# Kernel tuning notes

Hardware: AMD Instinct MI355X
Metric: run time of the kernel (lower is better)

The kernel has to match this reference:

```python
import jax, jax.numpy as jnp
import numpy as np

B, S, D, H, P = 2, 2048, 512, 8, 10  # batch, seq, d_model, heads, max_relative_position
DH = D // H
SCALE = float(np.sqrt(D))  # module uses sqrt(d_model) in relative branch


def _rel_indices(len_q, len_k, max_rel):
    rq = jnp.arange(len_q)
    rk = jnp.arange(len_k)
    dist = rk[None, :] - rq[:, None]
    return jnp.clip(dist, -max_rel, max_rel) + max_rel  # [len_q, len_k]


def setup_inputs() -> dict:
    key = jax.random.key(0)
    ks = jax.random.split(key, 12)
    init = lambda k, shp, s=0.02: (jax.random.normal(k, shp, dtype=jnp.float32) * s)
    return {
        "q": jax.random.normal(ks[0], (B, S, D), dtype=jnp.float32),
        "k": jax.random.normal(ks[1], (B, S, D), dtype=jnp.float32),
        "v": jax.random.normal(ks[2], (B, S, D), dtype=jnp.float32),
        "mask": jnp.ones((1, 1, S, S), dtype=jnp.int32),  # no-op in original (masked_fill result discarded)
        "Wq": init(ks[3], (D, D)), "bq": init(ks[4], (D,)),
        "Wk": init(ks[5], (D, D)), "bk": init(ks[6], (D,)),
        "Wv": init(ks[7], (D, D)), "bv": init(ks[8], (D,)),
        "W0": init(ks[9], (D, D)), "b0": init(ks[10], (D,)),
        "rel_k_table": init(ks[11], (2 * P + 1, DH), 0.02),
        "rel_v_table": init(jax.random.fold_in(key, 99), (2 * P + 1, DH), 0.02),
    }


def reference(q, k, v, mask, Wq, bq, Wk, bk, Wv, bv, W0, b0, rel_k_table, rel_v_table):
    # Projections (nn.Linear equivalent with weight stored as [in, out])
    query = q @ Wq + bq  # [B,S,D]
    key_ = k @ Wk + bk
    value = v @ Wv + bv

    qh = query.reshape(B, S, H, DH)  # [B,S,H,DH]
    kh = key_.reshape(B, S, H, DH)
    vh = value.reshape(B, S, H, DH)

    idx = _rel_indices(S, S, P)              # [S,S]
    rel_k = rel_k_table[idx]                 # [S,S,DH]
    rel_v = rel_v_table[idx]                 # [S,S,DH]

    normal_scores = jnp.einsum("bqhd,bkhd->bhqk", qh, kh)
    rel_scores = jnp.einsum("bqhd,qkd->bhqk", qh, rel_k)
    # NOTE: original relative branch applies NO softmax; mask is a no-op (masked_fill not in-place)
    scores = (normal_scores + rel_scores) / SCALE  # [B,H,S,S]

    weight1 = jnp.einsum("bhqk,bkhd->bhqd", scores, vh)
    weight2 = jnp.einsum("bhqk,qkd->bhqd", scores, rel_v)
    x = (weight1 + weight2).transpose(0, 2, 1, 3).reshape(B, S, D)
    return x @ W0 + b0
```

## Files before the change

kernel.cpp:

```cpp
#include <hip/hip_runtime.h>
#include <hip/hip_bf16.h>


typedef __attribute__((ext_vector_type(8)))  short  short8;
typedef __attribute__((ext_vector_type(4)))  short  short4v;
typedef __attribute__((ext_vector_type(4)))  int    int4v;
typedef __attribute__((ext_vector_type(16))) float  f32x16;
typedef __attribute__((ext_vector_type(8)))  __bf16 bf16x8;

#define DEV static __device__ __forceinline__

constexpr float INV_SCALE = 0.044194173824159216f;

DEV unsigned short f2bs(float f){ __hip_bfloat16 h = __float2bfloat16(f); unsigned short u; __builtin_memcpy(&u,&h,2); return u; }
DEV short f2b(float f){ return (short)f2bs(f); }
DEV int   pk2(float a, float b){ return (int)((unsigned)f2bs(a) | ((unsigned)f2bs(b) << 16)); }
DEV bf16x8 ld8s(const short* p){ return __builtin_bit_cast(bf16x8, *(const short8*)p); }
DEV f32x16 z16(){ f32x16 z;
#pragma unroll
  for (int i=0;i<16;++i) z[i]=0.f;
  return z; }
DEV f32x16 mfma32(bf16x8 a, bf16x8 b, f32x16 c){ return __builtin_amdgcn_mfma_f32_32x32x16_bf16(a,b,c,0,0,0); }

struct WtArgs { const float* W[4]; short* O[4]; };

__global__ __launch_bounds__(256) void wt_kernel(WtArgs args){
  const float* W = args.W[blockIdx.z];
  short* O = args.O[blockIdx.z];
  const int kt = blockIdx.x*64, nt = blockIdx.y*64;
  __shared__ float t[64][65];
  const int tid = threadIdx.x;
#pragma unroll
  for (int p=0;p<4;++p){
    int idx = p*1024 + tid*4; int r = idx>>6, c = idx&63;
    float4 v = *(const float4*)(W + (size_t)(kt+r)*512 + nt + c);
    t[r][c]=v.x; t[r][c+1]=v.y; t[r][c+2]=v.z; t[r][c+3]=v.w;
  }
  __syncthreads();
#pragma unroll
  for (int p=0;p<4;++p){
    int idx = p*1024 + tid*4; int n = idx>>6, k = idx&63;
    short4v o = { f2b(t[k][n]), f2b(t[k+1][n]), f2b(t[k+2][n]), f2b(t[k+3][n]) };
    *(short4v*)(O + (size_t)(nt+n)*512 + kt + k) = o;
  }
}

template<bool AF32, bool OUTB16>
DEV void gemm_body(const void* A, const short* BT, const float* bias, void* C,
                   int m0, int n0, short* Alds, short* Blds){
  const int tid = threadIdx.x, lane = tid&63, wid = tid>>6, lo5 = lane&31, hi = lane>>5;
  f32x16 acc0 = z16(), acc1 = z16();
  for (int kt=0; kt<8; ++kt){
    const int k0 = kt*64;
    __syncthreads();
    {
      const int rr = tid>>3, c = tid&7;
#pragma unroll
      for (int p=0;p<4;++p){
        int row = p*32 + rr;
        short8 v;
        if (AF32){
          const float* ap = (const float*)A + (size_t)(m0+row)*512 + k0 + c*8;
          float4 x = *(const float4*)ap; float4 y = *(const float4*)(ap+4);
          v = short8{ f2b(x.x),f2b(x.y),f2b(x.z),f2b(x.w), f2b(y.x),f2b(y.y),f2b(y.z),f2b(y.w) };
        } else {
          v = *(const short8*)((const short*)A + (size_t)(m0+row)*512 + k0 + c*8);
        }
        *(short8*)&Alds[row*64 + ((c ^ (row&7))*8)] = v;
      }
#pragma unroll
      for (int p=0;p<2;++p){
        int row = p*32 + rr;
        short8 v = *(const short8*)(BT + (size_t)(n0+row)*512 + k0 + c*8);
        *(short8*)&Blds[row*64 + ((c ^ (row&7))*8)] = v;
      }
    }
    __syncthreads();
#pragma unroll
    for (int da=0; da<4; ++da){
      const int arow = wid*32 + lo5;
      bf16x8 af = ld8s(&Alds[arow*64 + (((2*da+hi) ^ (arow&7))*8)]);
      const int b0r = lo5, b1r = 32+lo5;
      bf16x8 bf0 = ld8s(&Blds[b0r*64 + (((2*da+hi) ^ (b0r&7))*8)]);
      bf16x8 bf1 = ld8s(&Blds[b1r*64 + (((2*da+hi) ^ (b1r&7))*8)]);
      acc0 = mfma32(af, bf0, acc0);
      acc1 = mfma32(af, bf1, acc1);
    }
  }
  const float bv0 = bias[n0 + lo5], bv1 = bias[n0 + 32 + lo5];
#pragma unroll
  for (int r=0;r<16;++r){
    const int m = m0 + wid*32 + (r&3) + 8*(r>>2) + 4*hi;
    const float v0 = acc0[r] + bv0, v1 = acc1[r] + bv1;
    if (OUTB16){
      ((short*)C)[(size_t)m*512 + n0 + lo5]      = f2b(v0);
      ((short*)C)[(size_t)m*512 + n0 + 32 + lo5] = f2b(v1);
    } else {
      ((float*)C)[(size_t)m*512 + n0 + lo5]      = v0;
      ((float*)C)[(size_t)m*512 + n0 + 32 + lo5] = v1;
    }
  }
}

struct ProjArgs { const float* A[3]; const short* BT[3]; const float* bias[3]; short* C[3]; };

__global__ __launch_bounds__(256) void proj_gemm(ProjArgs args){
  __shared__ short Alds[128*64];
  __shared__ short Blds[64*64];
  const int z = blockIdx.z;
  gemm_body<true,true>(args.A[z], args.BT[z], args.bias[z], args.C[z],
                       blockIdx.x*128, blockIdx.y*64, Alds, Blds);
}

__global__ __launch_bounds__(256) void out_gemm(const short* A, const short* BT, const float* bias, float* C){
  __shared__ short Alds[128*64];
  __shared__ short Blds[64*64];
  gemm_body<false,false>(A, BT, bias, C, blockIdx.x*128, blockIdx.y*64, Alds, Blds);
}

__global__ __launch_bounds__(256) void vt_kernel(const short* Vp, short* Vt){
  const int bh = blockIdx.y, s0 = blockIdx.x*64;
  const int b = bh>>3, h = bh&7;
  __shared__ short t[64][72];
  const int tid = threadIdx.x;
#pragma unroll
  for (int p=0;p<2;++p){
    int row = p*32 + (tid>>3), cc = (tid&7)*8;
    short8 v = *(const short8*)(Vp + (size_t)(b*2048 + s0 + row)*512 + h*64 + cc);
#pragma unroll
    for (int i=0;i<8;++i) t[row][cc+i] = v[i];
  }
  __syncthreads();
#pragma unroll
  for (int p=0;p<2;++p){
    int d = p*32 + (tid>>3), sc = (tid&7)*8;
    short8 o;
#pragma unroll
    for (int i=0;i<8;++i) o[i] = t[sc+i][d];
    *(short8*)(Vt + ((size_t)bh*64 + d)*2048 + s0 + sc) = o;
  }
}

__global__ __launch_bounds__(256) void attn_kernel(const short* Qp, const short* Kp, const short* Vt,
                                                   const float* relk_g, const float* relv_g, float* slab){
  const int qt = blockIdx.x, bh = blockIdx.y, ks = blockIdx.z;
  const int b = bh>>3, h = bh&7;
  const int tid = threadIdx.x, lane = tid&63, wid = tid>>6, lo5 = lane&31, hi = lane>>5;
  const int q0 = qt*128, qw = q0 + wid*32;

  __shared__ short Klds[64*64];
  __shared__ short Vl[64*64];
  __shared__ float Rq[128*21];
  __shared__ short CS[128*32];
  __shared__ short RVT[64*32];

  for (int i=tid; i<2048; i+=256) ((int*)CS)[i] = 0;
  for (int i=tid; i<2048; i+=256){
    int d = i>>5, j = i&31;
    RVT[d*32 + (j ^ ((d&3)<<3))] = (j<21) ? f2b(relv_g[j*64+d]) : (short)0;
  }

  bf16x8 qf[4];
  {
    const short* Qrow = Qp + (size_t)(b*2048 + qw + lo5)*512 + h*64 + hi*8;
#pragma unroll
    for (int da=0;da<4;++da) qf[da] = ld8s(Qrow + da*16);
  }

  {
    f32x16 rq = z16();
    const int jr = lo5 <= 20 ? lo5 : 20;
    const float* rp = relk_g + jr*64 + hi*8;
#pragma unroll
    for (int da=0;da<4;++da){
      const float* p = rp + da*16;
      float4 x = *(const float4*)p; float4 y = *(const float4*)(p+4);
      short8 rb = { f2b(x.x),f2b(x.y),f2b(x.z),f2b(x.w), f2b(y.x),f2b(y.y),f2b(y.z),f2b(y.w) };
      rq = mfma32(qf[da], __builtin_bit_cast(bf16x8, rb), rq);
    }
    if (lo5 <= 20){
#pragma unroll
      for (int r=0;r<16;++r){
        int qoff = (r&3) + 8*(r>>2) + 4*hi;
        Rq[(wid*32 + qoff)*21 + lo5] = rq[r];
      }
    }
  }
  __syncthreads();

  const int qrow = wid*32 + lo5;
  const int qg = q0 + qrow;
  const float r0  = Rq[qrow*21 + 0];
  const float r20 = Rq[qrow*21 + 20];
  float bin0 = 0.f, bin20 = 0.f;
  f32x16 w1a = z16(), w1b = z16();

  const short* Kg = Kp + (size_t)b*2048*512 + h*64;
  const short* Vg = Vt + (size_t)bh*64*2048;

  for (int kt=0; kt<16; ++kt){
    const int k0 = ks*1024 + kt*64;
    __syncthreads();
    {
      const int rr = tid>>3, c = tid&7;
#pragma unroll
      for (int p=0;p<2;++p){
        int row = p*32 + rr;
        short8 v = *(const short8*)(Kg + (size_t)(k0+row)*512 + c*8);
        *(short8*)&Klds[row*64 + ((c ^ (row&7))*8)] = v;
      }
#pragma unroll
      for (int p=0;p<2;++p){
        int d = p*32 + rr;
        short8 v = *(const short8*)(Vg + (size_t)d*2048 + k0 + c*8);
        *(short8*)&Vl[d*64 + ((c ^ (d&7))*8)] = v;
      }
    }
    __syncthreads();

#pragma unroll
    for (int ksub=0; ksub<2; ++ksub){
      const int kb = k0 + ksub*32;
      f32x16 acc = z16();
#pragma unroll
      for (int da=0;da<4;++da){
        const int arow = ksub*32 + lo5;
        bf16x8 af = ld8s(&Klds[arow*64 + (((2*da+hi) ^ (arow&7))*8)]);
        acc = mfma32(af, qf[da], acc);
      }
      float s[16];
      if (kb + 31 <= qw - 10){
#pragma unroll
        for (int r=0;r<16;++r){ float sv = (acc[r] + r0)*INV_SCALE; bin0 += sv; s[r]=sv; }
      } else if (kb >= qw + 41){
#pragma unroll
        for (int r=0;r<16;++r){ float sv = (acc[r] + r20)*INV_SCALE; bin20 += sv; s[r]=sv; }
      } else {
#pragma unroll
        for (int r=0;r<16;++r){
          const int krow = kb + (r&3) + 8*(r>>2) + 4*hi;
          const int delta = krow - qg;
          float rel;
          if (delta <= -10) rel = r0;
          else if (delta >= 10) rel = r20;
          else rel = Rq[qrow*21 + delta + 10];
          const float sv = (acc[r] + rel)*INV_SCALE;
          if (delta <= -10) bin0 += sv;
          else if (delta >= 10) bin20 += sv;
          else CS[qrow*32 + ((delta+10) ^ ((qrow&3)<<3))] = f2b(sv);
          s[r] = sv;
        }
      }
      const int x0 = pk2(s[0],s[1]),   x1 = pk2(s[2],s[3]);
      const int y0 = pk2(s[4],s[5]),   y1 = pk2(s[6],s[7]);
      const int x2 = pk2(s[8],s[9]),   x3 = pk2(s[10],s[11]);
      const int y2 = pk2(s[12],s[13]), y3 = pk2(s[14],s[15]);
      const int x0s=__shfl_xor(x0,32,64), x1s=__shfl_xor(x1,32,64);
      const int y0s=__shfl_xor(y0,32,64), y1s=__shfl_xor(y1,32,64);
      const int x2s=__shfl_xor(x2,32,64), x3s=__shfl_xor(x3,32,64);
      const int y2s=__shfl_xor(y2,32,64), y3s=__shfl_xor(y3,32,64);
      const bool lo = (hi==0);
      int4v A0 = { lo?x0:y0s, lo?x1:y1s, lo?x0s:y0, lo?x1s:y1 };
      int4v A1 = { lo?x2:y2s, lo?x3:y3s, lo?x2s:y2, lo?x3s:y3 };
      const bf16x8 pa0 = __builtin_bit_cast(bf16x8, A0);
      const bf16x8 pa1 = __builtin_bit_cast(bf16x8, A1);
#pragma unroll
      for (int c=0;c<2;++c){
        const bf16x8 pa = c ? pa1 : pa0;
        const int chunk = ksub*4 + 2*c + hi;
        {
          const int d = lo5;
          bf16x8 vb = ld8s(&Vl[d*64 + ((chunk ^ (d&7))*8)]);
          w1a = mfma32(pa, vb, w1a);
        }
        {
          const int d = 32 + lo5;
          bf16x8 vb = ld8s(&Vl[d*64 + ((chunk ^ (d&7))*8)]);
          w1b = mfma32(pa, vb, w1b);
        }
      }
    }
  }

  bin0  += __shfl_xor(bin0, 32, 64);
  bin20 += __shfl_xor(bin20, 32, 64);
  if (hi == 0){
    CS[qrow*32 + (0  ^ ((qrow&3)<<3))] = f2b(bin0);
    CS[qrow*32 + (20 ^ ((qrow&3)<<3))] = f2b(bin20);
  }
  __syncthreads();

  f32x16 w2a = z16(), w2b = z16();
#pragma unroll
  for (int c2=0;c2<2;++c2){
    const int arow = wid*32 + lo5;
    bf16x8 cf  = ld8s(&CS[arow*32 + ((16*c2 + 8*hi) ^ ((arow&3)<<3))]);
    const int d0 = lo5, d1 = 32 + lo5;
    bf16x8 rv0 = ld8s(&RVT[d0*32 + ((16*c2 + 8*hi) ^ ((d0&3)<<3))]);
    bf16x8 rv1 = ld8s(&RVT[d1*32 + ((16*c2 + 8*hi) ^ ((d1&3)<<3))]);
    w2a = mfma32(cf, rv0, w2a);
    w2b = mfma32(cf, rv1, w2b);
  }

  float* sl = slab + (size_t)ks*16*2048*64 + (size_t)bh*2048*64;
#pragma unroll
  for (int r=0;r<16;++r){
    const int q = q0 + wid*32 + (r&3) + 8*(r>>2) + 4*hi;
    sl[(size_t)q*64 + lo5]      = w1a[r] + w2a[r];
    sl[(size_t)q*64 + 32 + lo5] = w1b[r] + w2b[r];
  }
}

__global__ __launch_bounds__(256) void combine_kernel(const float* s0, const float* s1, short* xb){
  const size_t i4 = ((size_t)blockIdx.x*256 + threadIdx.x)*4;
  float4 a = *(const float4*)(s0 + i4);
  float4 c = *(const float4*)(s1 + i4);
  const int bh = (int)(i4 >> 17);
  const int rem = (int)(i4 & 131071);
  const int s = rem >> 6, dh = rem & 63;
  const size_t xi = ((size_t)(bh>>3)*2048 + s)*512 + (bh&7)*64 + dh;
  short4v o = { f2b(a.x+c.x), f2b(a.y+c.y), f2b(a.z+c.z), f2b(a.w+c.w) };
  *(short4v*)(xb + xi) = o;
}

extern "C" void kernel_launch(void* const* d_in, const int* in_sizes, int n_in,
                              void* d_out, int out_size, void* d_ws, size_t ws_size,
                              hipStream_t stream) {
  (void)in_sizes; (void)n_in; (void)out_size; (void)ws_size;
  const float* q    = (const float*)d_in[0];
  const float* k    = (const float*)d_in[1];
  const float* v    = (const float*)d_in[2];
  const float* Wq   = (const float*)d_in[4];
  const float* bq   = (const float*)d_in[5];
  const float* Wk   = (const float*)d_in[6];
  const float* bk   = (const float*)d_in[7];
  const float* Wv   = (const float*)d_in[8];
  const float* bv   = (const float*)d_in[9];
  const float* W0   = (const float*)d_in[10];
  const float* b0   = (const float*)d_in[11];
  const float* relk = (const float*)d_in[12];
  const float* relv = (const float*)d_in[13];
  float* out = (float*)d_out;
  char* ws = (char*)d_ws;

  short* WTq = (short*)(ws);
  short* WTk = WTq + 512*512;
  short* WTv = WTk + 512*512;
  short* WT0 = WTv + 512*512;
  short* Qp  = (short*)(ws + ((size_t)2<<20));
  short* Kp  = (short*)(ws + ((size_t)6<<20));
  short* Vp  = (short*)(ws + ((size_t)10<<20));
  short* Vt  = (short*)(ws + ((size_t)14<<20));
  float* slab= (float*)(ws + ((size_t)18<<20));
  short* xb  = (short*)(ws + ((size_t)34<<20));

  WtArgs wa = { {Wq, Wk, Wv, W0}, {WTq, WTk, WTv, WT0} };
  wt_kernel<<<dim3(8,8,4), 256, 0, stream>>>(wa);

  ProjArgs pa = { {q, k, v}, {WTq, WTk, WTv}, {bq, bk, bv}, {Qp, Kp, Vp} };
  proj_gemm<<<dim3(32,8,3), 256, 0, stream>>>(pa);

  vt_kernel<<<dim3(32,16), 256, 0, stream>>>(Vp, Vt);

  attn_kernel<<<dim3(16,16,2), 256, 0, stream>>>(Qp, Kp, Vt, relk, relv, slab);

  combine_kernel<<<2048, 256, 0, stream>>>(slab, slab + (size_t)16*2048*64, xb);

  out_gemm<<<dim3(32,8), 256, 0, stream>>>(xb, WT0, b0, out);
}
```

Measured before the change: 92.82 us.

## Split attention keys four ways with register prefetch and bf16 partial slabs

Raises the key-dimension split of the attention kernel from two to four, launching 1024 blocks instead of 512 to fill more CUs. K/V tiles are now prefetched into registers one iteration ahead to overlap global loads with MFMA work, and launch bounds request 4 blocks per SM. Partial outputs are stored as bf16 instead of fp32 and the combine kernel sums four partials. This lowers precision of the partial sums slightly and adds more combine traffic per element, though bf16 halves the bytes.

After: 91.05 us. About the same (-1.9%).

```diff
diff --git a/kernel.cpp b/kernel.cpp
--- a/kernel.cpp
+++ b/kernel.cpp
@@ -14,6 +14,7 @@
 
 DEV unsigned short f2bs(float f){ __hip_bfloat16 h = __float2bfloat16(f); unsigned short u; __builtin_memcpy(&u,&h,2); return u; }
 DEV short f2b(float f){ return (short)f2bs(f); }
+DEV float b2f(short s){ unsigned u = ((unsigned)(unsigned short)s)<<16; float f; __builtin_memcpy(&f,&u,4); return f; }
 DEV int   pk2(float a, float b){ return (int)((unsigned)f2bs(a) | ((unsigned)f2bs(b) << 16)); }
 DEV bf16x8 ld8s(const short* p){ return __builtin_bit_cast(bf16x8, *(const short8*)p); }
 DEV f32x16 z16(){ f32x16 z;
@@ -141,8 +142,8 @@
   }
 }
 
-__global__ __launch_bounds__(256) void attn_kernel(const short* Qp, const short* Kp, const short* Vt,
-                                                   const float* relk_g, const float* relv_g, float* slab){
+__global__ __launch_bounds__(256,4) void attn_kernel(const short* Qp, const short* Kp, const short* Vt,
+                                                     const float* relk_g, const float* relv_g, short* slab){
   const int qt = blockIdx.x, bh = blockIdx.y, ks = blockIdx.z;
   const int b = bh>>3, h = bh&7;
   const int tid = threadIdx.x, lane = tid&63, wid = tid>>6, lo5 = lane&31, hi = lane>>5;
@@ -167,6 +168,19 @@
     for (int da=0;da<4;++da) qf[da] = ld8s(Qrow + da*16);
   }
 
+  const short* Kg = Kp + (size_t)b*2048*512 + h*64;
+  const short* Vg = Vt + (size_t)bh*64*2048;
+  const int rr = tid>>3, cc8 = tid&7;
+
+  short8 kreg0, kreg1, vreg0, vreg1;
+  {
+    const int k0 = ks*512;
+    kreg0 = *(const short8*)(Kg + (size_t)(k0+rr)*512 + cc8*8);
+    kreg1 = *(const short8*)(Kg + (size_t)(k0+32+rr)*512 + cc8*8);
+    vreg0 = *(const short8*)(Vg + (size_t)rr*2048 + k0 + cc8*8);
+    vreg1 = *(const short8*)(Vg + (size_t)(32+rr)*2048 + k0 + cc8*8);
+  }
+
   {
     f32x16 rq = z16();
     const int jr = lo5 <= 20 ? lo5 : 20;
@@ -186,37 +200,33 @@
       }
     }
   }
-  __syncthreads();
 
   const int qrow = wid*32 + lo5;
   const int qg = q0 + qrow;
+  __syncthreads();
   const float r0  = Rq[qrow*21 + 0];
   const float r20 = Rq[qrow*21 + 20];
   float bin0 = 0.f, bin20 = 0.f;
   f32x16 w1a = z16(), w1b = z16();
 
-  const short* Kg = Kp + (size_t)b*2048*512 + h*64;
-  const short* Vg = Vt + (size_t)bh*64*2048;
-
-  for (int kt=0; kt<16; ++kt){
-    const int k0 = ks*1024 + kt*64;
+  for (int kt=0; kt<8; ++kt){
+    const int k0 = ks*512 + kt*64;
     __syncthreads();
     {
-      const int rr = tid>>3, c = tid&7;
-#pragma unroll
-      for (int p=0;p<2;++p){
-        int row = p*32 + rr;
-        short8 v = *(const short8*)(Kg + (size_t)(k0+row)*512 + c*8);
-        *(short8*)&Klds[row*64 + ((c ^ (row&7))*8)] = v;
-      }
-#pragma unroll
-      for (int p=0;p<2;++p){
-        int d = p*32 + rr;
-        short8 v = *(const short8*)(Vg + (size_t)d*2048 + k0 + c*8);
-        *(short8*)&Vl[d*64 + ((c ^ (d&7))*8)] = v;
-      }
+      const int rowa = rr, rowb = 32 + rr;
+      *(short8*)&Klds[rowa*64 + ((cc8 ^ (rowa&7))*8)] = kreg0;
+      *(short8*)&Klds[rowb*64 + ((cc8 ^ (rowb&7))*8)] = kreg1;
+      *(short8*)&Vl[rowa*64 + ((cc8 ^ (rowa&7))*8)] = vreg0;
+      *(short8*)&Vl[rowb*64 + ((cc8 ^ (rowb&7))*8)] = vreg1;
     }
     __syncthreads();
+    if (kt < 7){
+      const int kn = k0 + 64;
+      kreg0 = *(const short8*)(Kg + (size_t)(kn+rr)*512 + cc8*8);
+      kreg1 = *(const short8*)(Kg + (size_t)(kn+32+rr)*512 + cc8*8);
+      vreg0 = *(const short8*)(Vg + (size_t)rr*2048 + kn + cc8*8);
+      vreg1 = *(const short8*)(Vg + (size_t)(32+rr)*2048 + kn + cc8*8);
+    }
 
 #pragma unroll
     for (int ksub=0; ksub<2; ++ksub){
@@ -302,25 +312,35 @@
     w2b = mfma32(cf, rv1, w2b);
   }
 
-  float* sl = slab + (size_t)ks*16*2048*64 + (size_t)bh*2048*64;
+  short* sl = slab + ((size_t)ks*16 + bh)*2048*64;
 #pragma unroll
   for (int r=0;r<16;++r){
     const int q = q0 + wid*32 + (r&3) + 8*(r>>2) + 4*hi;
-    sl[(size_t)q*64 + lo5]      = w1a[r] + w2a[r];
-    sl[(size_t)q*64 + 32 + lo5] = w1b[r] + w2b[r];
-  }
-}
-
-__global__ __launch_bounds__(256) void combine_kernel(const float* s0, const float* s1, short* xb){
-  const size_t i4 = ((size_t)blockIdx.x*256 + threadIdx.x)*4;
-  float4 a = *(const float4*)(s0 + i4);
-  float4 c = *(const float4*)(s1 + i4);
-  const int bh = (int)(i4 >> 17);
-  const int rem = (int)(i4 & 131071);
+    sl[(size_t)q*64 + lo5]      = f2b(w1a[r] + w2a[r]);
+    sl[(size_t)q*64 + 32 + lo5] = f2b(w1b[r] + w2b[r]);
+  }
+}
+
+__global__ __launch_bounds__(256) void combine_kernel(const short* slab, short* xb){
+  const size_t i8 = ((size_t)blockIdx.x*256 + threadIdx.x)*8;
+  const size_t SS = (size_t)16*2048*64;
+  float acc[8];
+#pragma unroll
+  for (int j=0;j<8;++j) acc[j]=0.f;
+#pragma unroll
+  for (int s4=0;s4<4;++s4){
+    short8 v = *(const short8*)(slab + s4*SS + i8);
+#pragma unroll
+    for (int j=0;j<8;++j) acc[j] += b2f(v[j]);
+  }
+  const int bh = (int)(i8 >> 17);
+  const int rem = (int)(i8 & 131071);
   const int s = rem >> 6, dh = rem & 63;
   const size_t xi = ((size_t)(bh>>3)*2048 + s)*512 + (bh&7)*64 + dh;
-  short4v o = { f2b(a.x+c.x), f2b(a.y+c.y), f2b(a.z+c.z), f2b(a.w+c.w) };
-  *(short4v*)(xb + xi) = o;
+  short8 o;
+#pragma unroll
+  for (int j=0;j<8;++j) o[j] = f2b(acc[j]);
+  *(short8*)(xb + xi) = o;
 }
 
 extern "C" void kernel_launch(void* const* d_in, const int* in_sizes, int n_in,
@@ -351,7 +371,7 @@
   short* Kp  = (short*)(ws + ((size_t)6<<20));
   short* Vp  = (short*)(ws + ((size_t)10<<20));
   short* Vt  = (short*)(ws + ((size_t)14<<20));
-  float* slab= (float*)(ws + ((size_t)18<<20));
+  short* slab= (short*)(ws + ((size_t)18<<20));
   short* xb  = (short*)(ws + ((size_t)34<<20));
 
   WtArgs wa = { {Wq, Wk, Wv, W0}, {WTq, WTk, WTv, WT0} };
@@ -362,9 +382,9 @@
 
   vt_kernel<<<dim3(32,16), 256, 0, stream>>>(Vp, Vt);
 
-  attn_kernel<<<dim3(16,16,2), 256, 0, stream>>>(Qp, Kp, Vt, relk, relv, slab);
-
-  combine_kernel<<<2048, 256, 0, stream>>>(slab, slab + (size_t)16*2048*64, xb);
+  attn_kernel<<<dim3(16,16,4), 256, 0, stream>>>(Qp, Kp, Vt, relk, relv, slab);
+
+  combine_kernel<<<1024, 256, 0, stream>>>(slab, xb);
 
   out_gemm<<<dim3(32,8), 256, 0, stream>>>(xb, WT0, b0, out);
 }
```
